# Performance work log

Measured on AMD Instinct MI355X. Metric: run time of the kernel, lower is better.

The kernel has to match this reference:

```python
import jax, jax.numpy as jnp
import numpy as np

# ---- static config (matches init_kwargs) ----
B, L, D, H, NC = 2, 4096, 256, 8, 3
TOP_N, R = 8, 32              # top_n, vicinity_radius
LS, LE = 1000, 3000           # label_start, label_end
NL = 2                        # n_cross_attn_layers
FF = 4 * D                    # ffn_expand * d_model
Q_MAX = 2 * TOP_N * (2 * R + 1)  # 1040
HD = D // H


def setup_inputs() -> dict:
    key = jax.random.key(0)
    ks = jax.random.split(key, 12)
    def rn(k, shape, s=0.05):
        return jax.random.normal(k, shape, jnp.float32) * s
    return {
        "encoder_output": jax.random.normal(ks[0], (B, L, D), jnp.float32),
        "coarse_logits": jax.random.normal(ks[1], (B, L, NC), jnp.float32),
        "ln_q_g": jnp.ones((NL, D), jnp.float32),
        "ln_q_b": jnp.zeros((NL, D), jnp.float32),
        "ln_kv_g": jnp.ones((NL, D), jnp.float32),
        "ln_kv_b": jnp.zeros((NL, D), jnp.float32),
        "Wq": rn(ks[2], (NL, D, D)), "bq": jnp.zeros((NL, D), jnp.float32),
        "Wk": rn(ks[3], (NL, D, D)), "bk": jnp.zeros((NL, D), jnp.float32),
        "Wv": rn(ks[4], (NL, D, D)), "bv": jnp.zeros((NL, D), jnp.float32),
        "Wo": rn(ks[5], (NL, D, D)), "bo": jnp.zeros((NL, D), jnp.float32),
        "ffn_g": jnp.ones((NL, D), jnp.float32),
        "ffn_b": jnp.zeros((NL, D), jnp.float32),
        "W1": rn(ks[6], (NL, D, FF)), "b1": jnp.zeros((NL, FF), jnp.float32),
        "W2": rn(ks[7], (NL, FF, D)), "b2": jnp.zeros((NL, D), jnp.float32),
        "head_W": rn(ks[8], (D, NC)), "head_b": jnp.zeros((NC,), jnp.float32),
    }


def _layer_norm(x, g, b, eps=1e-5):
    m = jnp.mean(x, axis=-1, keepdims=True)
    v = jnp.mean(jnp.square(x - m), axis=-1, keepdims=True)
    return (x - m) * jax.lax.rsqrt(v + eps) * g + b


def _select_vicinities(coarse_logits):
    # eval mode: no gumbel noise. Returns (vicinity_idx (B,Q_MAX) int32 with
    # sentinel L at pad/dup slots, q_pad_mask (B,Q_MAX) bool).
    lp = jax.nn.log_softmax(coarse_logits.astype(jnp.float32), axis=-1)
    pos = jnp.arange(L)
    region = (pos >= LS) & (pos < LE)
    acc = jnp.where(region, lp[..., 1], -jnp.inf)
    don = jnp.where(region, lp[..., 2], -jnp.inf)
    _, don_idx = jax.lax.top_k(don, TOP_N)
    _, acc_idx = jax.lax.top_k(acc, TOP_N)
    centers = jnp.concatenate([don_idx, acc_idx], axis=-1)        # (B, 2*TOP_N)
    offsets = jnp.arange(-R, R + 1)
    vic = jnp.clip(centers[:, :, None] + offsets, 0, L - 1).reshape(B, -1)
    s = jnp.sort(vic, axis=-1)
    is_first = jnp.concatenate(
        [jnp.ones((B, 1), bool), s[:, 1:] != s[:, :-1]], axis=-1)
    idx = jnp.where(is_first, s, L)  # sentinel L -> zero row of scratch
    return idx, is_first


def reference(encoder_output, coarse_logits, ln_q_g, ln_q_b, ln_kv_g, ln_kv_b,
              Wq, bq, Wk, bk, Wv, bv, Wo, bo, ffn_g, ffn_b, W1, b1, W2, b2,
              head_W, head_b):
    idx, mask = _select_vicinities(coarse_logits)      # torch.no_grad() region
    idx = jax.lax.stop_gradient(idx)
    mask = jax.lax.stop_gradient(mask)

    scratch = jnp.pad(encoder_output, ((0, 0), (0, 1), (0, 0)))   # (B, L+1, D)
    q_stream = jnp.take_along_axis(scratch, idx[:, :, None], axis=1)  # (B,Q,D)
    kv = encoder_output
    m3 = mask[:, :, None]

    for i in range(NL):
        q_in = _layer_norm(q_stream, ln_q_g[i], ln_q_b[i])
        kv_in = _layer_norm(kv, ln_kv_g[i], ln_kv_b[i])
        q = (q_in @ Wq[i] + bq[i]).reshape(B, Q_MAX, H, HD)
        k = (kv_in @ Wk[i] + bk[i]).reshape(B, L, H, HD)
        v = (kv_in @ Wv[i] + bv[i]).reshape(B, L, H, HD)
        scores = jnp.einsum('bqhd,bkhd->bhqk', q, k) / jnp.sqrt(
            jnp.float32(HD))
        attn = jax.nn.softmax(scores, axis=-1)
        ao = jnp.einsum('bhqk,bkhd->bqhd', attn, v).reshape(B, Q_MAX, D)
        q_stream = q_stream + ao @ Wo[i] + bo[i]
        q_stream = jnp.where(m3, q_stream, 0.0)
        h = _layer_norm(q_stream, ffn_g[i], ffn_b[i])
        h = jax.nn.gelu(h @ W1[i] + b1[i], approximate=False) @ W2[i] + b2[i]
        q_stream = jnp.where(m3, q_stream + h, 0.0)

    out_scratch = scratch.at[jnp.arange(B)[:, None], idx].set(q_stream)
    refined = out_scratch[:, :L]                                  # drop sentinel
    refined_logits = refined @ head_W + head_b                    # (B, L, 3)
    return refined_logits
```

## Files before the change

kernel.cpp:

```cpp
#include <hip/hip_runtime.h>
#include <cmath>

constexpr int B = 2, L = 4096, D = 256, H = 8, NC = 3;
constexpr int TOP_N = 8, R = 32;
constexpr int LS = 1000, LE = 3000;
constexpr int NL = 2;
constexpr int FF = 4 * D;
constexpr int Q_MAX = 2 * TOP_N * (2 * R + 1);
constexpr int HD = D / H;
constexpr int QROWS = B * Q_MAX;
constexpr int KVROWS = B * L;
constexpr int NQT = (Q_MAX + 31) / 32;
constexpr int NREG = LE - LS;
constexpr int NSPLIT = 8;
constexpr int KCHUNK = L / NSPLIT;
constexpr int NT = KCHUNK / 32;
constexpr int KVBLK = 8 * (KVROWS / 64);
constexpr int QBLK = 4 * ((QROWS + 63) / 64);
constexpr int TRBLK = NL * 192;
constexpr int LNBLK = KVROWS / 4;
constexpr int MRB32 = QROWS / 32;

typedef __attribute__((ext_vector_type(8))) short bf16x8;
typedef __attribute__((ext_vector_type(4))) float f32x4;
typedef __attribute__((ext_vector_type(4))) int i32x4;
typedef unsigned short u16;

union fr {
  bf16x8 h;
  i32x4 i;
};

__device__ __forceinline__ u16 f2bs(float f) {
  unsigned int u = __float_as_uint(f);
  unsigned int r = u + 0x7fffu + ((u >> 16) & 1u);
  return (u16)(r >> 16);
}
__device__ __forceinline__ float bs2f(u16 s) {
  return __uint_as_float(((unsigned int)s) << 16);
}
__device__ __forceinline__ float gelu_exact(float x) {
  return 0.5f * x * (1.f + erff(x * 0.70710678118654752440f));
}
__device__ __forceinline__ unsigned cvt_pk(float lo, float hi) {
  unsigned r;
  asm("v_cvt_pk_bf16_f32 %0, %1, %2" : "=v"(r) : "v"(lo), "v"(hi));
  return r;
}

#define GLL16(gsrc, ldst)                                                   \
  __builtin_amdgcn_global_load_lds(                                         \
      (const __attribute__((address_space(1))) unsigned int*)(gsrc),        \
      (__attribute__((address_space(3))) unsigned int*)(ldst), 16, 0, 0)

__device__ __forceinline__ void wave_ln_stats(float4 v, float& mean,
                                              float& rstd) {
  float s1 = v.x + v.y + v.z + v.w;
  float s2 = v.x * v.x + v.y * v.y + v.z * v.z + v.w * v.w;
#pragma unroll
  for (int off = 32; off; off >>= 1) {
    s1 += __shfl_xor(s1, off, 64);
    s2 += __shfl_xor(s2, off, 64);
  }
  mean = s1 * (1.f / D);
  float var = fmaxf(s2 * (1.f / D) - mean * mean, 0.f);
  rstd = rsqrtf(var + 1e-5f);
}

__global__ __launch_bounds__(256) void setup_kernel(
    const float* __restrict__ enc, const float* __restrict__ logits,
    const float* __restrict__ lnkvg, const float* __restrict__ lnkvb,
    const float* __restrict__ Wq_, const float* __restrict__ Wk_,
    const float* __restrict__ Wv_, const float* __restrict__ Wo_,
    const float* __restrict__ W1_, const float* __restrict__ W2_,
    u16* __restrict__ WT, u16* __restrict__ o0, u16* __restrict__ o1,
    int* __restrict__ idx_out, int* __restrict__ mask_out,
    int* __restrict__ inv_out) {
  int bid = blockIdx.x;
  int tid = threadIdx.x;
  const long DD = (long)D * D, DFF = (long)D * FF;
  const long LSTR = 4 * DD + 2 * DFF;

  if (bid < LNBLK) {
    long row = (long)bid * 4 + (tid >> 6);
    int lane = tid & 63;
    float4 v = *reinterpret_cast<const float4*>(enc + row * D + lane * 4);
    float mean, rstd;
    wave_ln_stats(v, mean, rstd);
    float n0 = (v.x - mean) * rstd, n1 = (v.y - mean) * rstd,
          n2 = (v.z - mean) * rstd, n3 = (v.w - mean) * rstd;
    int c = lane * 4;
    float4 g0 = *reinterpret_cast<const float4*>(lnkvg + c);
    float4 b0v = *reinterpret_cast<const float4*>(lnkvb + c);
    float4 g1 = *reinterpret_cast<const float4*>(lnkvg + D + c);
    float4 b1v = *reinterpret_cast<const float4*>(lnkvb + D + c);
    uint2 w0 = {cvt_pk(n0 * g0.x + b0v.x, n1 * g0.y + b0v.y),
                cvt_pk(n2 * g0.z + b0v.z, n3 * g0.w + b0v.w)};
    uint2 w1 = {cvt_pk(n0 * g1.x + b1v.x, n1 * g1.y + b1v.y),
                cvt_pk(n2 * g1.z + b1v.z, n3 * g1.w + b1v.w)};
    *reinterpret_cast<uint2*>(o0 + row * D + c) = w0;
    *reinterpret_cast<uint2*>(o1 + row * D + c) = w1;
    return;
  }

  if (bid < LNBLK + TRBLK) {
    __shared__ u16 T[64][65];
    int t = bid - LNBLK;
    int l = t / 192, r = t % 192;
    const float* src;
    long dbase;
    int K_, N_, kt, nt;
    if (r < 64) {
      int which = r >> 4, sub = r & 15;
      kt = sub >> 2;
      nt = sub & 3;
      K_ = 256;
      N_ = 256;
      src = (which == 0 ? Wk_ : which == 1 ? Wv_ : which == 2 ? Wq_ : Wo_) +
            (long)l * DD;
      dbase = (long)l * LSTR + (long)which * DD;
    } else if (r < 128) {
      int sub = r - 64;
      kt = sub >> 4;
      nt = sub & 15;
      K_ = 256;
      N_ = 1024;
      src = W1_ + (long)l * DFF;
      dbase = (long)l * LSTR + 4 * DD;
    } else {
      int sub = r - 128;
      kt = sub >> 2;
      nt = sub & 3;
      K_ = 1024;
      N_ = 256;
      src = W2_ + (long)l * DFF;
      dbase = (long)l * LSTR + 4 * DD + DFF;
    }
    int k0 = kt * 64, n0 = nt * 64;
    {
      int kr = tid >> 2, c16 = (tid & 3) * 16;
      const float* sp = src + (long)(k0 + kr) * N_ + n0 + c16;
#pragma unroll
      for (int i = 0; i < 4; ++i) {
        float4 v = *reinterpret_cast<const float4*>(sp + 4 * i);
        T[kr][c16 + 4 * i + 0] = f2bs(v.x);
        T[kr][c16 + 4 * i + 1] = f2bs(v.y);
        T[kr][c16 + 4 * i + 2] = f2bs(v.z);
        T[kr][c16 + 4 * i + 3] = f2bs(v.w);
      }
    }
    __syncthreads();
    {
      int nr = tid >> 2, kc = (tid & 3) * 16;
      u16 tmp[16];
#pragma unroll
      for (int j = 0; j < 16; ++j) tmp[j] = T[kc + j][nr];
      u16* dp = WT + dbase + (long)(n0 + nr) * K_ + k0 + kc;
      *reinterpret_cast<bf16x8*>(dp) = *reinterpret_cast<const bf16x8*>(&tmp[0]);
      *reinterpret_cast<bf16x8*>(dp + 8) =
          *reinterpret_cast<const bf16x8*>(&tmp[8]);
    }
    return;
  }

  {
    int b = bid - LNBLK - TRBLK;
    int w = tid >> 6, lane = tid & 63;
    __shared__ float candv[4][8];
    __shared__ int candi[4][8];
    __shared__ int centers[2 * TOP_N];
    __shared__ unsigned present[L / 32];
    __shared__ int offs[128];
    __shared__ int wtot[2];

    float vd[8], va[8];
#pragma unroll
    for (int j = 0; j < 8; ++j) {
      int p = tid + j * 256;
      if (p < NREG) {
        const float* lg = logits + ((long)b * L + LS + p) * NC;
        float x0 = lg[0], x1 = lg[1], x2 = lg[2];
        float m = fmaxf(x0, fmaxf(x1, x2));
        float lse = m + logf(expf(x0 - m) + expf(x1 - m) + expf(x2 - m));
        vd[j] = x2 - lse;
        va[j] = x1 - lse;
      } else {
        vd[j] = -INFINITY;
        va[j] = -INFINITY;
      }
    }
    if (tid < 128) present[tid] = 0;
    for (int j = tid; j < L; j += 256) inv_out[(long)b * L + j] = -1;

    for (int sel = 0; sel < 2; ++sel) {
      float v[8];
#pragma unroll
      for (int j = 0; j < 8; ++j) v[j] = (sel == 0) ? vd[j] : va[j];
#pragma unroll
      for (int r = 0; r < TOP_N; ++r) {
        float mv = v[0];
        int mp = tid;
#pragma unroll
        for (int j = 1; j < 8; ++j) {
          int pj = tid + j * 256;
          if (v[j] > mv) { mv = v[j]; mp = pj; }
        }
#pragma unroll
        for (int off = 32; off; off >>= 1) {
          float ov = __shfl_xor(mv, off, 64);
          int oi = __shfl_xor(mp, off, 64);
          if (ov > mv || (ov == mv && oi < mp)) { mv = ov; mp = oi; }
        }
#pragma unroll
        for (int j = 0; j < 8; ++j)
          if (tid + j * 256 == mp) v[j] = -INFINITY;
        if (lane == 0) { candv[w][r] = mv; candi[w][r] = mp; }
      }
      __syncthreads();
      if (tid < 64) {
        float c = (tid < 32) ? candv[tid >> 3][tid & 7] : -INFINITY;
        int ci = (tid < 32) ? candi[tid >> 3][tid & 7] : 0x7fffffff;
#pragma unroll
        for (int r = 0; r < TOP_N; ++r) {
          float mv = c;
          int mi = ci;
#pragma unroll
          for (int off = 32; off; off >>= 1) {
            float ov = __shfl_xor(mv, off, 64);
            int oi = __shfl_xor(mi, off, 64);
            if (ov > mv || (ov == mv && oi < mi)) { mv = ov; mi = oi; }
          }
          if (ci == mi) c = -INFINITY;
          if (tid == 0) centers[sel * TOP_N + r] = LS + mi;
        }
      }
      __syncthreads();
    }

    for (int j = tid; j < Q_MAX; j += 256) {
      int c = centers[j / (2 * R + 1)];
      int off = j % (2 * R + 1) - R;
      int v2 = c + off;
      v2 = v2 < 0 ? 0 : (v2 > L - 1 ? L - 1 : v2);
      atomicOr(&present[v2 >> 5], 1u << (v2 & 31));
    }
    __syncthreads();

    int cnt = (tid < 128) ? __popc(present[tid]) : 0;
    if (tid < 128) {
      int x = cnt;
#pragma unroll
      for (int off = 1; off < 64; off <<= 1) {
        int o = __shfl_up(x, off, 64);
        if ((tid & 63) >= off) x += o;
      }
      if ((tid & 63) == 63) wtot[tid >> 6] = x;
      offs[tid] = x - cnt;
    }
    __syncthreads();
    int total = wtot[0] + wtot[1];
    if (tid < 128) {
      int base = offs[tid] + ((tid >= 64) ? wtot[0] : 0);
      unsigned mword = present[tid];
      while (mword) {
        int i = __ffs(mword) - 1;
        mword &= mword - 1;
        int pos = tid * 32 + i;
        idx_out[b * Q_MAX + base] = pos;
        mask_out[b * Q_MAX + base] = 1;
        inv_out[(long)b * L + pos] = b * Q_MAX + base;
        ++base;
      }
    }
    for (int j = total + tid; j < Q_MAX; j += 256) {
      idx_out[b * Q_MAX + j] = L;
      mask_out[b * Q_MAX + j] = 0;
    }
  }
}

__global__ __launch_bounds__(256) void gather_ln(
    const float* __restrict__ enc, const int* __restrict__ idx,
    float* __restrict__ q_stream, u16* __restrict__ q_ln,
    const float* __restrict__ gg, const float* __restrict__ bb) {
  int row = blockIdx.x * 4 + (threadIdx.x >> 6);
  int lane = threadIdx.x & 63;
  int b = row / Q_MAX;
  int p = idx[row];
  int c = lane * 4;
  float4 v = {0.f, 0.f, 0.f, 0.f};
  if (p < L) v = *reinterpret_cast<const float4*>(enc + ((long)b * L + p) * D + c);
  *reinterpret_cast<float4*>(q_stream + (long)row * D + c) = v;
  float mean, rstd;
  wave_ln_stats(v, mean, rstd);
  float4 g = *reinterpret_cast<const float4*>(gg + c);
  float4 bt = *reinterpret_cast<const float4*>(bb + c);
  uint2 w = {cvt_pk((v.x - mean) * rstd * g.x + bt.x,
                    (v.y - mean) * rstd * g.y + bt.y),
             cvt_pk((v.z - mean) * rstd * g.z + bt.z,
                    (v.w - mean) * rstd * g.w + bt.w)};
  *reinterpret_cast<uint2*>(q_ln + (long)row * D + c) = w;
}

__global__ __launch_bounds__(256) void ln_bf16(
    const float* __restrict__ in, u16* __restrict__ out,
    const float* __restrict__ gg, const float* __restrict__ bb) {
  long row = (long)blockIdx.x * 4 + (threadIdx.x >> 6);
  int lane = threadIdx.x & 63;
  int c = lane * 4;
  float4 v = *reinterpret_cast<const float4*>(in + row * D + c);
  float mean, rstd;
  wave_ln_stats(v, mean, rstd);
  float4 g = *reinterpret_cast<const float4*>(gg + c);
  float4 bt = *reinterpret_cast<const float4*>(bb + c);
  uint2 w = {cvt_pk((v.x - mean) * rstd * g.x + bt.x,
                    (v.y - mean) * rstd * g.y + bt.y),
             cvt_pk((v.z - mean) * rstd * g.z + bt.z,
                    (v.w - mean) * rstd * g.w + bt.w)};
  *reinterpret_cast<uint2*>(out + row * D + c) = w;
}

template <int EPI>
__global__ __launch_bounds__(256) void gemm_mfma(
    const u16* __restrict__ A, const u16* __restrict__ BT,
    const float* __restrict__ bias, void* __restrict__ Cv,
    const float* __restrict__ resid, const int* __restrict__ mask, int M,
    int N, int K) {
  __shared__ short As[64][40];
  __shared__ short Bs[64][40];
  int bm = blockIdx.y * 64, bn = blockIdx.x * 64;
  int tid = threadIdx.x;
  int lane = tid & 63, w = tid >> 6;
  int g = lane >> 4, li = lane & 15;
  int wr = w >> 1, wc = w & 1;
  f32x4 acc[2][2] = {};

  int srow = tid >> 2, skc = (tid & 3) * 8;
  for (int k0 = 0; k0 < K; k0 += 32) {
    {
      int grow = bm + srow;
      bf16x8 av = {};
      if (grow < M)
        av = *reinterpret_cast<const bf16x8*>(A + (long)grow * K + k0 + skc);
      *reinterpret_cast<bf16x8*>(&As[srow][skc]) = av;
      bf16x8 bv = *reinterpret_cast<const bf16x8*>(
          BT + (long)(bn + srow) * K + k0 + skc);
      *reinterpret_cast<bf16x8*>(&Bs[srow][skc]) = bv;
    }
    __syncthreads();
    bf16x8 a0 = *reinterpret_cast<const bf16x8*>(&As[wr * 32 + li][g * 8]);
    bf16x8 a1 = *reinterpret_cast<const bf16x8*>(&As[wr * 32 + 16 + li][g * 8]);
    bf16x8 b0 = *reinterpret_cast<const bf16x8*>(&Bs[wc * 32 + li][g * 8]);
    bf16x8 b1 = *reinterpret_cast<const bf16x8*>(&Bs[wc * 32 + 16 + li][g * 8]);
    acc[0][0] = __builtin_amdgcn_mfma_f32_16x16x32_bf16(a0, b0, acc[0][0], 0, 0, 0);
    acc[0][1] = __builtin_amdgcn_mfma_f32_16x16x32_bf16(a0, b1, acc[0][1], 0, 0, 0);
    acc[1][0] = __builtin_amdgcn_mfma_f32_16x16x32_bf16(a1, b0, acc[1][0], 0, 0, 0);
    acc[1][1] = __builtin_amdgcn_mfma_f32_16x16x32_bf16(a1, b1, acc[1][1], 0, 0, 0);
    __syncthreads();
  }

#pragma unroll
  for (int mr = 0; mr < 2; ++mr)
#pragma unroll
    for (int nr = 0; nr < 2; ++nr)
#pragma unroll
      for (int r = 0; r < 4; ++r) {
        int row = bm + wr * 32 + mr * 16 + g * 4 + r;
        int col = bn + wc * 32 + nr * 16 + li;
        if (row >= M) continue;
        float v = acc[mr][nr][r] + bias[col];
        if (EPI == 1) v = gelu_exact(v);
        if (EPI == 2) {
          v += resid[(long)row * N + col];
          v = mask[row] ? v : 0.f;
          ((float*)Cv)[(long)row * N + col] = v;
        } else {
          ((u16*)Cv)[(long)row * N + col] = f2bs(v);
        }
      }
}

__global__ __launch_bounds__(128) void gemm_mfma32(
    const u16* __restrict__ A, const u16* __restrict__ BT,
    const float* __restrict__ bias, float* __restrict__ Cv,
    const float* __restrict__ resid, const int* __restrict__ mask, int M,
    int N, int K) {
  __shared__ short As[32][40];
  __shared__ short Bs[64][40];
  int bm = blockIdx.y * 32, bn = blockIdx.x * 64;
  int tid = threadIdx.x;
  int lane = tid & 63, w = tid >> 6;
  int g = lane >> 4, li = lane & 15;
  f32x4 acc[2][2] = {};

  int srow = tid >> 2, skc = (tid & 3) * 8;
  for (int k0 = 0; k0 < K; k0 += 32) {
    {
      bf16x8 av = *reinterpret_cast<const bf16x8*>(
          A + (long)(bm + srow) * K + k0 + skc);
      *reinterpret_cast<bf16x8*>(&As[srow][skc]) = av;
      bf16x8 bv0 = *reinterpret_cast<const bf16x8*>(
          BT + (long)(bn + srow) * K + k0 + skc);
      *reinterpret_cast<bf16x8*>(&Bs[srow][skc]) = bv0;
      bf16x8 bv1 = *reinterpret_cast<const bf16x8*>(
          BT + (long)(bn + 32 + srow) * K + k0 + skc);
      *reinterpret_cast<bf16x8*>(&Bs[32 + srow][skc]) = bv1;
    }
    __syncthreads();
    bf16x8 a0 = *reinterpret_cast<const bf16x8*>(&As[li][g * 8]);
    bf16x8 a1 = *reinterpret_cast<const bf16x8*>(&As[16 + li][g * 8]);
    bf16x8 b0 = *reinterpret_cast<const bf16x8*>(&Bs[w * 32 + li][g * 8]);
    bf16x8 b1 = *reinterpret_cast<const bf16x8*>(&Bs[w * 32 + 16 + li][g * 8]);
    acc[0][0] = __builtin_amdgcn_mfma_f32_16x16x32_bf16(a0, b0, acc[0][0], 0, 0, 0);
    acc[0][1] = __builtin_amdgcn_mfma_f32_16x16x32_bf16(a0, b1, acc[0][1], 0, 0, 0);
    acc[1][0] = __builtin_amdgcn_mfma_f32_16x16x32_bf16(a1, b0, acc[1][0], 0, 0, 0);
    acc[1][1] = __builtin_amdgcn_mfma_f32_16x16x32_bf16(a1, b1, acc[1][1], 0, 0, 0);
    __syncthreads();
  }

#pragma unroll
  for (int mr = 0; mr < 2; ++mr)
#pragma unroll
    for (int nr = 0; nr < 2; ++nr)
#pragma unroll
      for (int r = 0; r < 4; ++r) {
        int row = bm + mr * 16 + g * 4 + r;
        int col = bn + w * 32 + nr * 16 + li;
        if (row >= M) continue;
        float v = acc[mr][nr][r] + bias[col] + resid[(long)row * N + col];
        v = mask[row] ? v : 0.f;
        Cv[(long)row * N + col] = v;
      }
}

__global__ __launch_bounds__(256) void gemm_proj(
    const u16* __restrict__ Akv, const u16* __restrict__ Aq,
    const u16* __restrict__ WTbase, const float* __restrict__ biasK,
    const float* __restrict__ biasV, const float* __restrict__ biasQ,
    u16* __restrict__ Kh, u16* __restrict__ Vh, u16* __restrict__ Qb) {
  __shared__ short As[64][40];
  __shared__ short Bs[64][40];
  __shared__ u16 Ct[64][72];
  int bid = blockIdx.x;
  int tid = threadIdx.x;
  int lane = tid & 63, w = tid >> 6;
  int g = lane >> 4, li = lane & 15;
  int wr = w >> 1, wc = w & 1;
  f32x4 acc[2][2] = {};
  const long DD = (long)D * D;

  bool isKV = bid < KVBLK;
  int bm, bn, M;
  const u16* A;
  const u16* BT;
  if (isKV) {
    bn = (bid & 7) * 64;
    bm = (bid >> 3) * 64;
    M = KVROWS;
    A = Akv;
    BT = WTbase;
  } else {
    int qb = bid - KVBLK;
    bn = (qb & 3) * 64;
    bm = (qb >> 2) * 64;
    M = QROWS;
    A = Aq;
    BT = WTbase + 2 * DD;
  }

  int srow = tid >> 2, skc = (tid & 3) * 8;
  for (int k0 = 0; k0 < D; k0 += 32) {
    {
      int grow = bm + srow;
      bf16x8 av = {};
      if (grow < M)
        av = *reinterpret_cast<const bf16x8*>(A + (long)grow * D + k0 + skc);
      *reinterpret_cast<bf16x8*>(&As[srow][skc]) = av;
      bf16x8 bv = *reinterpret_cast<const bf16x8*>(
          BT + (long)(bn + srow) * D + k0 + skc);
      *reinterpret_cast<bf16x8*>(&Bs[srow][skc]) = bv;
    }
    __syncthreads();
    bf16x8 a0 = *reinterpret_cast<const bf16x8*>(&As[wr * 32 + li][g * 8]);
    bf16x8 a1 = *reinterpret_cast<const bf16x8*>(&As[wr * 32 + 16 + li][g * 8]);
    bf16x8 b0 = *reinterpret_cast<const bf16x8*>(&Bs[wc * 32 + li][g * 8]);
    bf16x8 b1 = *reinterpret_cast<const bf16x8*>(&Bs[wc * 32 + 16 + li][g * 8]);
    acc[0][0] = __builtin_amdgcn_mfma_f32_16x16x32_bf16(a0, b0, acc[0][0], 0, 0, 0);
    acc[0][1] = __builtin_amdgcn_mfma_f32_16x16x32_bf16(a0, b1, acc[0][1], 0, 0, 0);
    acc[1][0] = __builtin_amdgcn_mfma_f32_16x16x32_bf16(a1, b0, acc[1][0], 0, 0, 0);
    acc[1][1] = __builtin_amdgcn_mfma_f32_16x16x32_bf16(a1, b1, acc[1][1], 0, 0, 0);
    __syncthreads();
  }

  if (!isKV) {
#pragma unroll
    for (int mr = 0; mr < 2; ++mr)
#pragma unroll
      for (int nr = 0; nr < 2; ++nr)
#pragma unroll
        for (int r = 0; r < 4; ++r) {
          int row = bm + wr * 32 + mr * 16 + g * 4 + r;
          int col = bn + wc * 32 + nr * 16 + li;
          if (row >= M) continue;
          Qb[(long)row * D + col] = f2bs(acc[mr][nr][r] + biasQ[col]);
        }
  } else if (bn < 256) {
#pragma unroll
    for (int mr = 0; mr < 2; ++mr)
#pragma unroll
      for (int nr = 0; nr < 2; ++nr)
#pragma unroll
        for (int r = 0; r < 4; ++r) {
          int rowL = wr * 32 + mr * 16 + g * 4 + r;
          int colL = wc * 32 + nr * 16 + li;
          Ct[rowL][colL] = f2bs(acc[mr][nr][r] + biasK[bn + colL]);
        }
    __syncthreads();
#pragma unroll
    for (int p = 0; p < 2; ++p) {
      int rowL = (tid >> 3) + p * 32;
      int c8 = (tid & 7) * 8;
      int grow = bm + rowL;
      int b2 = grow >> 12, key = grow & (L - 1);
      int gcol = bn + c8;
      int hh = gcol >> 5, dd = gcol & (HD - 1);
      int cst = (dd >> 3) ^ ((key >> 1) & 3);
      u16* dst = Kh + (((long)(b2 * H + hh) * L + key) * 32 + (cst << 3));
      *reinterpret_cast<bf16x8*>(dst) =
          *reinterpret_cast<const bf16x8*>(&Ct[rowL][c8]);
    }
  } else {
    int vbn = bn - 256;
#pragma unroll
    for (int mr = 0; mr < 2; ++mr)
#pragma unroll
      for (int nr = 0; nr < 2; ++nr)
#pragma unroll
        for (int r = 0; r < 4; ++r) {
          int rowL = wr * 32 + mr * 16 + g * 4 + r;
          int colL = wc * 32 + nr * 16 + li;
          Ct[colL][rowL] = f2bs(acc[mr][nr][r] + biasV[vbn + colL]);
        }
    __syncthreads();
    int b2 = bm >> 12;
#pragma unroll
    for (int p = 0; p < 2; ++p) {
      int colL = (tid >> 3) + p * 32;
      int rem = tid & 7;
      int kb = rem >> 2, k8 = (rem & 3) * 8;
      int gcol = vbn + colL;
      int hh = gcol >> 5, dd = gcol & (HD - 1);
      int kb32 = ((bm & (L - 1)) >> 5) + kb;
      int j = (k8 >> 2) ^ ((dd >> 1) & 6);
      u16* dst = Vh + (((long)(b2 * H + hh) * (L / 32) + kb32) * 1024 +
                       dd * 32 + (j << 2));
      *reinterpret_cast<bf16x8*>(dst) =
          *reinterpret_cast<const bf16x8*>(&Ct[colL][kb * 32 + k8]);
    }
  }
}

constexpr int POOLSZ = NSPLIT * 32 * 33 * 4 + NSPLIT * 32 * 4;

__global__ __launch_bounds__(512) void attn_mfma(
    const u16* __restrict__ Qb, const u16* __restrict__ Kh,
    const u16* __restrict__ Vh, u16* __restrict__ AO) {
  __shared__ alignas(16) char pool[POOLSZ];
  int i = blockIdx.x;
  int xcd = i & 7, slot = i >> 3;
  int bh = (xcd << 1) | (slot >= NQT ? 1 : 0);
  int qt = (slot >= NQT) ? slot - NQT : slot;
  int h = bh & 7;
  int b = bh >> 3;
  int tid = threadIdx.x, w = tid >> 6, lane = tid & 63;
  int g = lane >> 4, li = lane & 15;

  fr qf0, qf1;
  {
    const float QSC = 0.25509836048f;
#pragma unroll
    for (int qb = 0; qb < 2; ++qb) {
      int qrow = qt * 32 + qb * 16 + li;
      if (qrow >= Q_MAX) qrow = Q_MAX - 1;
      bf16x8 raw = *reinterpret_cast<const bf16x8*>(
          Qb + ((long)(b * Q_MAX + qrow)) * D + h * HD + g * 8);
      fr& qf = qb ? qf1 : qf0;
#pragma unroll
      for (int j = 0; j < 4; ++j)
        qf.i[j] = (int)cvt_pk(bs2f((u16)raw[2 * j]) * QSC,
                              bs2f((u16)raw[2 * j + 1]) * QSC);
    }
  }

  f32x4 acc00 = {}, acc01 = {}, acc10 = {}, acc11 = {};
  float den0 = 0.f, den1 = 0.f;
  const f32x4 z = {};

  const u16* kbase = Kh + ((long)(b * H + h) * L) * HD;
  const u16* vbase = Vh + ((long)(b * H + h) * L) * HD;
  int kstart = w * KCHUNK;
  char* wbase = pool + w * 4096;

  int s_li = (li >> 1) & 3;
  int t_li = (li >> 1) & 6;
  int kof0 = li * 32 + ((g ^ s_li) << 3);
  int kof1 = (16 + li) * 32 + ((g ^ s_li) << 3);
  int va0o = li * 32 + ((g ^ t_li) << 2);
  int vb0o = li * 32 + (((4 + g) ^ t_li) << 2);
  int va1o = (16 + li) * 32 + ((g ^ t_li) << 2);
  int vb1o = (16 + li) * 32 + (((4 + g) ^ t_li) << 2);

  {
    const u16* ks = kbase + (long)kstart * HD + lane * 8;
    const u16* vs = vbase + (long)kstart * HD + lane * 8;
    u16* lk = (u16*)wbase;
    GLL16(ks, lk);
    GLL16(ks + 512, lk + 512);
    GLL16(vs, lk + 1024);
    GLL16(vs + 512, lk + 1536);
  }

  for (int t = 0; t < NT; ++t) {
    const u16* kl = (const u16*)wbase;
    const u16* vl = kl + 1024;

    asm volatile("s_waitcnt vmcnt(2)" ::: "memory");
    __builtin_amdgcn_sched_barrier(0);
    fr kf0, kf1;
    kf0.h = *reinterpret_cast<const bf16x8*>(kl + kof0);
    kf1.h = *reinterpret_cast<const bf16x8*>(kl + kof1);
    asm volatile("" ::"v"(kf0.i[0]), "v"(kf0.i[1]), "v"(kf0.i[2]),
                 "v"(kf0.i[3]), "v"(kf1.i[0]), "v"(kf1.i[1]), "v"(kf1.i[2]),
                 "v"(kf1.i[3]));
    asm volatile("s_waitcnt lgkmcnt(0)" ::: "memory");
    __builtin_amdgcn_sched_barrier(0);
    if (t + 1 < NT) {
      const u16* ks = kbase + (long)(kstart + (t + 1) * 32) * HD + lane * 8;
      u16* lk = (u16*)wbase;
      GLL16(ks, lk);
      GLL16(ks + 512, lk + 512);
    }

    __builtin_amdgcn_s_setprio(1);
    f32x4 s00 = __builtin_amdgcn_mfma_f32_16x16x32_bf16(kf0.h, qf0.h, z, 0, 0, 0);
    f32x4 s10 = __builtin_amdgcn_mfma_f32_16x16x32_bf16(kf1.h, qf0.h, z, 0, 0, 0);
    f32x4 s01 = __builtin_amdgcn_mfma_f32_16x16x32_bf16(kf0.h, qf1.h, z, 0, 0, 0);
    f32x4 s11 = __builtin_amdgcn_mfma_f32_16x16x32_bf16(kf1.h, qf1.h, z, 0, 0, 0);
    __builtin_amdgcn_s_setprio(0);

    float p00[4], p10[4], p01[4], p11[4];
#pragma unroll
    for (int r = 0; r < 4; ++r) {
      p00[r] = exp2f(s00[r]);
      p10[r] = exp2f(s10[r]);
      p01[r] = exp2f(s01[r]);
      p11[r] = exp2f(s11[r]);
      den0 += p00[r] + p10[r];
      den1 += p01[r] + p11[r];
    }
    fr pf0, pf1;
    pf0.i[0] = (int)cvt_pk(p00[0], p00[1]);
    pf0.i[1] = (int)cvt_pk(p00[2], p00[3]);
    pf0.i[2] = (int)cvt_pk(p10[0], p10[1]);
    pf0.i[3] = (int)cvt_pk(p10[2], p10[3]);
    pf1.i[0] = (int)cvt_pk(p01[0], p01[1]);
    pf1.i[1] = (int)cvt_pk(p01[2], p01[3]);
    pf1.i[2] = (int)cvt_pk(p11[0], p11[1]);
    pf1.i[3] = (int)cvt_pk(p11[2], p11[3]);

    if (t + 1 < NT)
      asm volatile("s_waitcnt vmcnt(2)" ::: "memory");
    else
      asm volatile("s_waitcnt vmcnt(0)" ::: "memory");
    __builtin_amdgcn_sched_barrier(0);
    uint2 va0 = *reinterpret_cast<const uint2*>(vl + va0o);
    uint2 vb0 = *reinterpret_cast<const uint2*>(vl + vb0o);
    uint2 va1 = *reinterpret_cast<const uint2*>(vl + va1o);
    uint2 vb1 = *reinterpret_cast<const uint2*>(vl + vb1o);
    asm volatile("" ::"v"(va0.x), "v"(va0.y), "v"(vb0.x), "v"(vb0.y),
                 "v"(va1.x), "v"(va1.y), "v"(vb1.x), "v"(vb1.y));
    asm volatile("s_waitcnt lgkmcnt(0)" ::: "memory");
    __builtin_amdgcn_sched_barrier(0);
    if (t + 1 < NT) {
      const u16* vs = vbase + (long)(kstart + (t + 1) * 32) * HD + lane * 8;
      u16* lk = (u16*)wbase;
      GLL16(vs, lk + 1024);
      GLL16(vs + 512, lk + 1536);
    }

    fr v0, v1;
    v0.i = (i32x4){(int)va0.x, (int)va0.y, (int)vb0.x, (int)vb0.y};
    v1.i = (i32x4){(int)va1.x, (int)va1.y, (int)vb1.x, (int)vb1.y};
    __builtin_amdgcn_s_setprio(1);
    acc00 = __builtin_amdgcn_mfma_f32_16x16x32_bf16(v0.h, pf0.h, acc00, 0, 0, 0);
    acc01 = __builtin_amdgcn_mfma_f32_16x16x32_bf16(v0.h, pf1.h, acc01, 0, 0, 0);
    acc10 = __builtin_amdgcn_mfma_f32_16x16x32_bf16(v1.h, pf0.h, acc10, 0, 0, 0);
    acc11 = __builtin_amdgcn_mfma_f32_16x16x32_bf16(v1.h, pf1.h, acc11, 0, 0, 0);
    __builtin_amdgcn_s_setprio(0);
  }

  den0 += __shfl_xor(den0, 16, 64);
  den0 += __shfl_xor(den0, 32, 64);
  den1 += __shfl_xor(den1, 16, 64);
  den1 += __shfl_xor(den1, 32, 64);

  __syncthreads();
  float(*accs)[32][33] = (float(*)[32][33])pool;
  float(*dsh)[32] = (float(*)[32])(pool + NSPLIT * 32 * 33 * 4);
#pragma unroll
  for (int r = 0; r < 4; ++r) {
    accs[w][g * 4 + r][li] = acc00[r];
    accs[w][g * 4 + r][16 + li] = acc01[r];
    accs[w][16 + g * 4 + r][li] = acc10[r];
    accs[w][16 + g * 4 + r][16 + li] = acc11[r];
  }
  if (g == 0) {
    dsh[w][li] = den0;
    dsh[w][16 + li] = den1;
  }
  __syncthreads();

  int q = tid >> 4, dp = tid & 15;
  float Den = 0.f, o0 = 0.f, o1 = 0.f;
#pragma unroll
  for (int ww = 0; ww < NSPLIT; ++ww) {
    Den += dsh[ww][q];
    o0 += accs[ww][2 * dp][q];
    o1 += accs[ww][2 * dp + 1][q];
  }
  float inv = 1.f / Den;
  int qrow = qt * 32 + q;
  if (qrow < Q_MAX) {
    unsigned pk = cvt_pk(o0 * inv, o1 * inv);
    *reinterpret_cast<unsigned*>(
        AO + ((long)(b * Q_MAX + qrow)) * D + h * HD + 2 * dp) = pk;
  }
}

__global__ __launch_bounds__(256) void head_kernel(
    const float* __restrict__ enc, const float* __restrict__ q_stream,
    const int* __restrict__ inv, const float* __restrict__ hW,
    const float* __restrict__ hb, float* __restrict__ out) {
  int row = blockIdx.x * 4 + (threadIdx.x >> 6);
  int lane = threadIdx.x & 63;
  int slot = inv[row];
  const float* src =
      (slot >= 0) ? (q_stream + (long)slot * D) : (enc + (long)row * D);
  const float4 a = *reinterpret_cast<const float4*>(src + lane * 4);
  float c0 = 0.f, c1 = 0.f, c2 = 0.f;
  const float av[4] = {a.x, a.y, a.z, a.w};
#pragma unroll
  for (int i = 0; i < 4; ++i) {
    int k = lane * 4 + i;
    c0 += av[i] * hW[k * 3];
    c1 += av[i] * hW[k * 3 + 1];
    c2 += av[i] * hW[k * 3 + 2];
  }
#pragma unroll
  for (int off = 32; off; off >>= 1) {
    c0 += __shfl_down(c0, off, 64);
    c1 += __shfl_down(c1, off, 64);
    c2 += __shfl_down(c2, off, 64);
  }
  if (lane == 0) {
    out[(long)row * 3] = c0 + hb[0];
    out[(long)row * 3 + 1] = c1 + hb[1];
    out[(long)row * 3 + 2] = c2 + hb[2];
  }
}

extern "C" void kernel_launch(void* const* d_in, const int* in_sizes, int n_in,
                              void* d_out, int out_size, void* d_ws,
                              size_t ws_size, hipStream_t stream) {
  const float* enc = (const float*)d_in[0];
  const float* clog = (const float*)d_in[1];
  const float* ln_q_g = (const float*)d_in[2];
  const float* ln_q_b = (const float*)d_in[3];
  const float* ln_kv_g = (const float*)d_in[4];
  const float* ln_kv_b = (const float*)d_in[5];
  const float* Wq = (const float*)d_in[6];
  const float* bq = (const float*)d_in[7];
  const float* Wk = (const float*)d_in[8];
  const float* bk = (const float*)d_in[9];
  const float* Wv = (const float*)d_in[10];
  const float* bv = (const float*)d_in[11];
  const float* Wo = (const float*)d_in[12];
  const float* bo = (const float*)d_in[13];
  const float* ffn_g = (const float*)d_in[14];
  const float* ffn_b = (const float*)d_in[15];
  const float* W1 = (const float*)d_in[16];
  const float* b1 = (const float*)d_in[17];
  const float* W2 = (const float*)d_in[18];
  const float* b2 = (const float*)d_in[19];
  const float* head_W = (const float*)d_in[20];
  const float* head_b = (const float*)d_in[21];
  float* out = (float*)d_out;

  char* ws = (char*)d_ws;
  float* q_stream = (float*)ws;            ws += (long)QROWS * D * 4;
  u16* kvl0 = (u16*)ws;                    ws += (long)KVROWS * D * 2;
  u16* kvl1 = (u16*)ws;                    ws += (long)KVROWS * D * 2;
  u16* Khbuf = (u16*)ws;                   ws += (long)B * H * L * HD * 2;
  u16* Vhbuf = (u16*)ws;                   ws += (long)B * H * L * HD * 2;
  u16* q_ln = (u16*)ws;                    ws += (long)QROWS * D * 2;
  u16* Qbuf = (u16*)ws;                    ws += (long)QROWS * D * 2;
  u16* AObuf = (u16*)ws;                   ws += (long)QROWS * D * 2;
  u16* H1buf = (u16*)ws;                   ws += (long)QROWS * FF * 2;
  u16* WT = (u16*)ws;                      ws += (long)NL * (4 * D * D + 2 * D * FF) * 2;
  int* idxbuf = (int*)ws;                  ws += QROWS * 4;
  int* maskbuf = (int*)ws;                 ws += QROWS * 4;
  int* invbuf = (int*)ws;                  ws += (long)B * L * 4;

  const long DD = (long)D * D, DFF = (long)D * FF;
  const long LSTR = 4 * DD + 2 * DFF;

  setup_kernel<<<LNBLK + TRBLK + B, 256, 0, stream>>>(
      enc, clog, ln_kv_g, ln_kv_b, Wq, Wk, Wv, Wo, W1, W2, WT, kvl0, kvl1,
      idxbuf, maskbuf, invbuf);
  gather_ln<<<QROWS / 4, 256, 0, stream>>>(enc, idxbuf, q_stream, q_ln,
                                           ln_q_g, ln_q_b);

  for (int l = 0; l < NL; ++l) {
    u16* base = WT + l * LSTR;
    u16* kv_ln = (l == 0) ? kvl0 : kvl1;

    if (l > 0)
      ln_bf16<<<QROWS / 4, 256, 0, stream>>>(q_stream, q_ln, ln_q_g + l * D,
                                             ln_q_b + l * D);

    gemm_proj<<<KVBLK + QBLK, 256, 0, stream>>>(
        kv_ln, q_ln, base, bk + l * D, bv + l * D, bq + l * D, Khbuf, Vhbuf,
        Qbuf);

    attn_mfma<<<B * H * NQT, 512, 0, stream>>>(Qbuf, Khbuf, Vhbuf, AObuf);

    gemm_mfma32<<<dim3(D / 64, MRB32), 128, 0, stream>>>(
        AObuf, base + 3 * DD, bo + l * D, q_stream, q_stream, maskbuf, QROWS,
        D, D);

    ln_bf16<<<QROWS / 4, 256, 0, stream>>>(q_stream, q_ln, ffn_g + l * D,
                                           ffn_b + l * D);
    dim3 gF1(FF / 64, (QROWS + 63) / 64);
    gemm_mfma<1><<<gF1, 256, 0, stream>>>(q_ln, base + 4 * DD, b1 + l * FF,
                                          (void*)H1buf, nullptr, nullptr,
                                          QROWS, FF, D);
    gemm_mfma32<<<dim3(D / 64, MRB32), 128, 0, stream>>>(
        H1buf, base + 4 * DD + DFF, b2 + l * D, q_stream, q_stream, maskbuf,
        QROWS, D, FF);
  }

  head_kernel<<<KVROWS / 4, 256, 0, stream>>>(enc, q_stream, invbuf, head_W,
                                              head_b, out);
}
```

Before: 210.1 us.

## Double-buffer gemm_proj tiles with direct global-to-LDS loads and XOR swizzle

The projection GEMM's K loop now loads A and B tiles straight from global memory into LDS via GLL16 into two alternating buffers. The next K-slice is prefetched while MFMAs run on the current one, and there is one barrier per iteration instead of two. An XOR swizzle on the 8-element column groups replaces the padded LDS rows to avoid bank conflicts, and s_setprio raises priority around the MFMA burst. The row bounds check on A is dropped, so the last Q tile may read past QROWS unless the buffer is padded.

After: 207.5 us. No clear change (-1.2%).

```diff
diff --git a/kernel.cpp b/kernel.cpp
--- a/kernel.cpp
+++ b/kernel.cpp
@@ -438,8 +438,8 @@
     const u16* __restrict__ WTbase, const float* __restrict__ biasK,
     const float* __restrict__ biasV, const float* __restrict__ biasQ,
     u16* __restrict__ Kh, u16* __restrict__ Vh, u16* __restrict__ Qb) {
-  __shared__ short As[64][40];
-  __shared__ short Bs[64][40];
+  __shared__ alignas(16) u16 Asb[2][2048];
+  __shared__ alignas(16) u16 Bsb[2][2048];
   __shared__ u16 Ct[64][72];
   int bid = blockIdx.x;
   int tid = threadIdx.x;
@@ -468,29 +468,46 @@
     BT = WTbase + 2 * DD;
   }
 
-  int srow = tid >> 2, skc = (tid & 3) * 8;
-  for (int k0 = 0; k0 < D; k0 += 32) {
-    {
-      int grow = bm + srow;
-      bf16x8 av = {};
-      if (grow < M)
-        av = *reinterpret_cast<const bf16x8*>(A + (long)grow * D + k0 + skc);
-      *reinterpret_cast<bf16x8*>(&As[srow][skc]) = av;
-      bf16x8 bv = *reinterpret_cast<const bf16x8*>(
-          BT + (long)(bn + srow) * D + k0 + skc);
-      *reinterpret_cast<bf16x8*>(&Bs[srow][skc]) = bv;
-    }
-    __syncthreads();
-    bf16x8 a0 = *reinterpret_cast<const bf16x8*>(&As[wr * 32 + li][g * 8]);
-    bf16x8 a1 = *reinterpret_cast<const bf16x8*>(&As[wr * 32 + 16 + li][g * 8]);
-    bf16x8 b0 = *reinterpret_cast<const bf16x8*>(&Bs[wc * 32 + li][g * 8]);
-    bf16x8 b1 = *reinterpret_cast<const bf16x8*>(&Bs[wc * 32 + 16 + li][g * 8]);
+  int srow = w * 16 + (lane >> 2);
+  int sgo = (((lane & 3) ^ ((srow >> 1) & 3)) << 3);
+  const u16* aRow = A + (long)(bm + srow) * D + sgo;
+  const u16* bRow = BT + (long)(bn + srow) * D + sgo;
+
+  int ra = wr * 32 + li;
+  int ofA0 = ra * 32 + ((g ^ ((ra >> 1) & 3)) << 3);
+  int ofA1 = ofA0 + 16 * 32;
+  int rb = wc * 32 + li;
+  int ofB0 = rb * 32 + ((g ^ ((rb >> 1) & 3)) << 3);
+  int ofB1 = ofB0 + 16 * 32;
+
+  GLL16(aRow, Asb[0] + w * 512);
+  GLL16(bRow, Bsb[0] + w * 512);
+
+#pragma unroll 1
+  for (int ks = 0; ks < D / 32; ++ks) {
+    asm volatile("s_waitcnt lgkmcnt(0)" ::: "memory");
+    asm volatile("s_waitcnt vmcnt(0)" ::: "memory");
+    __builtin_amdgcn_sched_barrier(0);
+    __builtin_amdgcn_s_barrier();
+    if (ks + 1 < D / 32) {
+      GLL16(aRow + (ks + 1) * 32, Asb[(ks + 1) & 1] + w * 512);
+      GLL16(bRow + (ks + 1) * 32, Bsb[(ks + 1) & 1] + w * 512);
+    }
+    const u16* Ab = Asb[ks & 1];
+    const u16* Bb = Bsb[ks & 1];
+    bf16x8 a0 = *reinterpret_cast<const bf16x8*>(Ab + ofA0);
+    bf16x8 a1 = *reinterpret_cast<const bf16x8*>(Ab + ofA1);
+    bf16x8 b0 = *reinterpret_cast<const bf16x8*>(Bb + ofB0);
+    bf16x8 b1 = *reinterpret_cast<const bf16x8*>(Bb + ofB1);
+    __builtin_amdgcn_s_setprio(1);
     acc[0][0] = __builtin_amdgcn_mfma_f32_16x16x32_bf16(a0, b0, acc[0][0], 0, 0, 0);
     acc[0][1] = __builtin_amdgcn_mfma_f32_16x16x32_bf16(a0, b1, acc[0][1], 0, 0, 0);
     acc[1][0] = __builtin_amdgcn_mfma_f32_16x16x32_bf16(a1, b0, acc[1][0], 0, 0, 0);
     acc[1][1] = __builtin_amdgcn_mfma_f32_16x16x32_bf16(a1, b1, acc[1][1], 0, 0, 0);
-    __syncthreads();
-  }
+    __builtin_amdgcn_s_setprio(0);
+  }
+  asm volatile("s_waitcnt lgkmcnt(0)" ::: "memory");
+  __builtin_amdgcn_s_barrier();
 
   if (!isKV) {
 #pragma unroll
```
